# Kernel optimization log

Measured on AMD Instinct MI355X. Metric: run time of the kernel, lower is better.

## Reference

```python
import jax, jax.numpy as jnp
import numpy as np

C_IN = 64
C_QK = C_IN // 8  # 8


def setup_inputs() -> dict:
    key = jax.random.key(0)
    ks = jax.random.split(key, 8)
    B, C, D, H, W = 2, C_IN, 8, 32, 32
    x = jax.random.normal(ks[0], (B, C, D, H, W), dtype=jnp.float32)
    s = 1.0 / np.sqrt(C)
    Wq = jax.random.normal(ks[1], (C_QK, C), dtype=jnp.float32) * s
    bq = jax.random.normal(ks[2], (C_QK,), dtype=jnp.float32) * 0.01
    Wk = jax.random.normal(ks[3], (C_QK, C), dtype=jnp.float32) * s
    bk = jax.random.normal(ks[4], (C_QK,), dtype=jnp.float32) * 0.01
    Wv = jax.random.normal(ks[5], (C, C), dtype=jnp.float32) * s
    bv = jax.random.normal(ks[6], (C,), dtype=jnp.float32) * 0.01
    gamma = jax.random.normal(ks[7], (1,), dtype=jnp.float32) * 0.1
    return {"x": x, "Wq": Wq, "bq": bq, "Wk": Wk, "bk": bk,
            "Wv": Wv, "bv": bv, "gamma": gamma}


def reference(x, Wq, bq, Wk, bk, Wv, bv, gamma):
    B, C, D, H, W = x.shape
    N = D * H * W
    xf = x.reshape(B, C, N)  # flatten spatial dims (D,H,W order)
    # 1x1x1 conv3d == per-position channel matmul
    q = jnp.einsum('oc,bcn->bno', Wq, xf) + bq            # [B, N, Cqk]
    k = jnp.einsum('oc,bcn->bon', Wk, xf) + bk[:, None]   # [B, Cqk, N]
    v = jnp.einsum('oc,bcn->bon', Wv, xf) + bv[:, None]   # [B, C, N]
    energy = jnp.einsum('bnc,bcm->bnm', q, k)             # [B, N, N] (unscaled)
    attn = jax.nn.softmax(energy, axis=-1)
    # out[b,c,m] = sum_n v[b,c,n] * attn[b,m,n]  (bmm with attention^T)
    out = jnp.einsum('bcn,bmn->bcm', v, attn)
    out = out.reshape(B, C, D, H, W)
    return gamma[0] * out + x
```

## Files before the change

### kernel.cpp

```cpp
#include <hip/hip_runtime.h>
#include <hip/hip_bf16.h>
#include <math.h>

#define NPOS 8192
#define CIN 64
#define CQK 8
#define NB 2
#define LOG2E 1.4426950408889634f
#define SOFF 16.0f
#define EXP2_SCALE 8388608.0f
#define EXP2_BIAS  1065173216.0f

typedef __attribute__((ext_vector_type(8))) short bf16x8;
typedef __attribute__((ext_vector_type(16))) float f32x16;

__device__ __forceinline__ unsigned short f2bf(float f) {
  union { float f; unsigned int u; } a; a.f = f;
  unsigned int r = a.u + 0x7FFFu + ((a.u >> 16) & 1u);
  return (unsigned short)(r >> 16);
}

__global__ __launch_bounds__(256, 2) void qkv_proj(
    const float* __restrict__ x,
    const float* __restrict__ Wq, const float* __restrict__ bq,
    const float* __restrict__ Wk, const float* __restrict__ bk,
    const float* __restrict__ Wv, const float* __restrict__ bv,
    unsigned short* __restrict__ Qb, unsigned short* __restrict__ Kb,
    unsigned short* __restrict__ VB) {
  __shared__ float sWq[CQK * CIN], sWk[CQK * CIN], sWv[CIN * CIN], sb[2 * CQK + CIN];
  __shared__ unsigned short sV[32][66];
  int t = threadIdx.x;
  for (int i = t; i < CQK * CIN; i += 256) { sWq[i] = Wq[i] * LOG2E; sWk[i] = Wk[i]; }
  for (int i = t; i < CIN * CIN; i += 256) sWv[i] = Wv[i];
  if (t < CQK) sb[t] = bq[t] * LOG2E;
  if (t >= CQK && t < 2 * CQK) sb[t] = bk[t - CQK];
  if (t >= 2 * CQK && t < 2 * CQK + CIN) sb[t] = bv[t - 2 * CQK];
  __syncthreads();

  int p_loc = t & 31, grp = t >> 5;
  int gid = blockIdx.x * 32 + p_loc;
  int b = gid >> 13;
  int n = gid & (NPOS - 1);
  const float* xp = x + (size_t)b * CIN * NPOS + n;
  float xv[CIN];
#pragma unroll
  for (int c = 0; c < CIN; ++c) xv[c] = xp[(size_t)c * NPOS];

  {
    int o = grp;
    float aq = sb[o], ak = sb[CQK + o];
    const float4* wq4 = (const float4*)&sWq[o * CIN];
    const float4* wk4 = (const float4*)&sWk[o * CIN];
#pragma unroll
    for (int c4 = 0; c4 < 16; ++c4) {
      float4 wq = wq4[c4], wk = wk4[c4];
      float x0 = xv[4 * c4], x1 = xv[4 * c4 + 1], x2 = xv[4 * c4 + 2], x3 = xv[4 * c4 + 3];
      aq += wq.x * x0 + wq.y * x1 + wq.z * x2 + wq.w * x3;
      ak += wk.x * x0 + wk.y * x1 + wk.z * x2 + wk.w * x3;
    }
    Qb[(size_t)gid * CQK + o] = f2bf(aq);
    Kb[(size_t)gid * CQK + o] = f2bf(ak);
  }
#pragma unroll
  for (int oo = 0; oo < 8; ++oo) {
    int o = grp * 8 + oo;
    float av = sb[2 * CQK + o];
    const float4* wv4 = (const float4*)&sWv[o * CIN];
#pragma unroll
    for (int c4 = 0; c4 < 16; ++c4) {
      float4 w = wv4[c4];
      av += w.x * xv[4 * c4] + w.y * xv[4 * c4 + 1] + w.z * xv[4 * c4 + 2] + w.w * xv[4 * c4 + 3];
    }
    sV[p_loc][o] = f2bf(av);
  }
  __syncthreads();

  {
    int gid0 = blockIdx.x * 32;
    int bb = gid0 >> 13;
    int jb = (gid0 & (NPOS - 1)) >> 5;
    int f = t >> 6;
    int ln = t & 63;
    int ch = ((f >> 1) << 5) + (ln & 31);
    int w0 = ((f & 1) << 4) + (((ln >> 5) & 1) << 2);
    union { unsigned short s[8]; bf16x8 v; } ou;
#pragma unroll
    for (int i = 0; i < 8; ++i) {
      int p = w0 + (i & 3) + (((i >> 2) & 1) << 3);
      ou.s[i] = sV[p][ch];
    }
    *reinterpret_cast<bf16x8*>(
        VB + (((size_t)bb * 256 + jb) * 2048 + (size_t)f * 512 + ln * 8)) = ou.v;
  }
}

__global__ __launch_bounds__(512, 2) void flash_attn(
    const unsigned short* __restrict__ Qb, const unsigned short* __restrict__ Kb,
    const unsigned short* __restrict__ VB, const float* __restrict__ x,
    const float* __restrict__ gamma, float* __restrict__ out) {
  int tid = threadIdx.x;
  int wave = tid >> 6, lane = tid & 63;
  int qcol = lane & 31, hi = lane >> 5;
  int blk = blockIdx.x;
  int b = blk >> 7, qt = blk & 127;
  int qbase = qt * 64;

  bf16x8 qfrag0, qfrag1;
#pragma unroll
  for (int i = 0; i < 8; ++i) { qfrag0[i] = 0; qfrag1[i] = 0; }
  if (!hi) {
    qfrag0 = *reinterpret_cast<const bf16x8*>(Qb + ((size_t)b * NPOS + qbase + qcol) * CQK);
    qfrag1 = *reinterpret_cast<const bf16x8*>(Qb + ((size_t)b * NPOS + qbase + 32 + qcol) * CQK);
  }

  bf16x8 ones;
#pragma unroll
  for (int i = 0; i < 8; ++i) ones[i] = (short)0x3F80;

  f32x16 z;
#pragma unroll
  for (int i = 0; i < 16; ++i) z[i] = -SOFF;
  f32x16 accA0, accB0, accA1, accB1;
  f32x16 accL0, accL1;
#pragma unroll
  for (int i = 0; i < 16; ++i) {
    accA0[i] = 0.f; accB0[i] = 0.f; accA1[i] = 0.f; accB1[i] = 0.f;
    accL0[i] = 0.f; accL1[i] = 0.f;
  }

  const unsigned short* Kp = Kb + (size_t)b * NPOS * CQK;
  const bf16x8* Vt = reinterpret_cast<const bf16x8*>(VB + (size_t)b * 256 * 2048);

  int jb0 = wave << 5;
  bf16x8 kcur = *reinterpret_cast<const bf16x8*>(Kp + ((size_t)(jb0 << 5) + qcol) * CQK);

  for (int tt = 0; tt < 32; ++tt) {
    const bf16x8* tile = Vt + (size_t)(jb0 + tt) * 256;
    bf16x8 va0 = tile[lane];
    bf16x8 va1 = tile[64 + lane];
    bf16x8 vb0 = tile[128 + lane];
    bf16x8 vb1 = tile[192 + lane];

    f32x16 S0 = __builtin_amdgcn_mfma_f32_32x32x16_bf16(kcur, qfrag0, z, 0, 0, 0);
    f32x16 S1 = __builtin_amdgcn_mfma_f32_32x32x16_bf16(kcur, qfrag1, z, 0, 0, 0);

    int jn = jb0 + ((tt + 1) & 31);
    bf16x8 knx = *reinterpret_cast<const bf16x8*>(Kp + ((size_t)(jn << 5) + qcol) * CQK);

    unsigned int pk0[8], pk1[8];
#pragma unroll
    for (int jj = 0; jj < 8; ++jj) {
      unsigned int ua = (unsigned int)fmaf(S0[2 * jj],     EXP2_SCALE, EXP2_BIAS);
      unsigned int ub = (unsigned int)fmaf(S0[2 * jj + 1], EXP2_SCALE, EXP2_BIAS);
      unsigned int uc = (unsigned int)fmaf(S1[2 * jj],     EXP2_SCALE, EXP2_BIAS);
      unsigned int ud = (unsigned int)fmaf(S1[2 * jj + 1], EXP2_SCALE, EXP2_BIAS);
      pk0[jj] = __builtin_amdgcn_perm(ub, ua, 0x07060302u);
      pk1[jj] = __builtin_amdgcn_perm(ud, uc, 0x07060302u);
    }

    union { unsigned int ui[4]; bf16x8 v; } PA00, PA10, PA01, PA11;
    PA00.ui[0] = pk0[0]; PA00.ui[1] = pk0[1]; PA00.ui[2] = pk0[2]; PA00.ui[3] = pk0[3];
    PA10.ui[0] = pk0[4]; PA10.ui[1] = pk0[5]; PA10.ui[2] = pk0[6]; PA10.ui[3] = pk0[7];
    PA01.ui[0] = pk1[0]; PA01.ui[1] = pk1[1]; PA01.ui[2] = pk1[2]; PA01.ui[3] = pk1[3];
    PA11.ui[0] = pk1[4]; PA11.ui[1] = pk1[5]; PA11.ui[2] = pk1[6]; PA11.ui[3] = pk1[7];

    accA0 = __builtin_amdgcn_mfma_f32_32x32x16_bf16(va0, PA00.v, accA0, 0, 0, 0);
    accA0 = __builtin_amdgcn_mfma_f32_32x32x16_bf16(va1, PA10.v, accA0, 0, 0, 0);
    accB0 = __builtin_amdgcn_mfma_f32_32x32x16_bf16(vb0, PA00.v, accB0, 0, 0, 0);
    accB0 = __builtin_amdgcn_mfma_f32_32x32x16_bf16(vb1, PA10.v, accB0, 0, 0, 0);
    accA1 = __builtin_amdgcn_mfma_f32_32x32x16_bf16(va0, PA01.v, accA1, 0, 0, 0);
    accA1 = __builtin_amdgcn_mfma_f32_32x32x16_bf16(va1, PA11.v, accA1, 0, 0, 0);
    accB1 = __builtin_amdgcn_mfma_f32_32x32x16_bf16(vb0, PA01.v, accB1, 0, 0, 0);
    accB1 = __builtin_amdgcn_mfma_f32_32x32x16_bf16(vb1, PA11.v, accB1, 0, 0, 0);
    accL0 = __builtin_amdgcn_mfma_f32_32x32x16_bf16(ones, PA00.v, accL0, 0, 0, 0);
    accL0 = __builtin_amdgcn_mfma_f32_32x32x16_bf16(ones, PA10.v, accL0, 0, 0, 0);
    accL1 = __builtin_amdgcn_mfma_f32_32x32x16_bf16(ones, PA01.v, accL1, 0, 0, 0);
    accL1 = __builtin_amdgcn_mfma_f32_32x32x16_bf16(ones, PA11.v, accL1, 0, 0, 0);

    kcur = knx;
  }

  __shared__ float sL[8][64];
  __shared__ float sLinv[64];
  __shared__ float sacc[64][68];
  if (!hi) { sL[wave][qcol] = accL0[0]; sL[wave][32 + qcol] = accL1[0]; }
  __syncthreads();
  if (tid < 64) {
    float L = 0.f;
#pragma unroll
    for (int w2 = 0; w2 < 8; ++w2) L += sL[w2][tid];
    sLinv[tid] = 1.0f / L;
  }

  for (int w2 = 0; w2 < 8; ++w2) {
    __syncthreads();
    if (wave == w2) {
#pragma unroll
      for (int k = 0; k < 4; ++k) {
        int c0 = (k << 3) + (hi << 2);
        float4 cA0 = make_float4(accA0[4 * k], accA0[4 * k + 1], accA0[4 * k + 2], accA0[4 * k + 3]);
        float4 cB0 = make_float4(accB0[4 * k], accB0[4 * k + 1], accB0[4 * k + 2], accB0[4 * k + 3]);
        float4 cA1 = make_float4(accA1[4 * k], accA1[4 * k + 1], accA1[4 * k + 2], accA1[4 * k + 3]);
        float4 cB1 = make_float4(accB1[4 * k], accB1[4 * k + 1], accB1[4 * k + 2], accB1[4 * k + 3]);
        float4* pA0 = (float4*)&sacc[qcol][c0];
        float4* pB0 = (float4*)&sacc[qcol][c0 + 32];
        float4* pA1 = (float4*)&sacc[32 + qcol][c0];
        float4* pB1 = (float4*)&sacc[32 + qcol][c0 + 32];
        if (w2 == 0) { *pA0 = cA0; *pB0 = cB0; *pA1 = cA1; *pB1 = cB1; }
        else {
          float4 a = *pA0, bb = *pB0, c = *pA1, d = *pB1;
          a.x += cA0.x; a.y += cA0.y; a.z += cA0.z; a.w += cA0.w;
          bb.x += cB0.x; bb.y += cB0.y; bb.z += cB0.z; bb.w += cB0.w;
          c.x += cA1.x; c.y += cA1.y; c.z += cA1.z; c.w += cA1.w;
          d.x += cB1.x; d.y += cB1.y; d.z += cB1.z; d.w += cB1.w;
          *pA0 = a; *pB0 = bb; *pA1 = c; *pB1 = d;
        }
      }
    }
  }
  __syncthreads();

  float g = gamma[0];
  for (int i = tid; i < CIN * 64; i += 512) {
    int c = i >> 6, q = i & 63;
    size_t idx = ((size_t)b * CIN + c) * NPOS + qbase + q;
    out[idx] = g * sacc[q][c] * sLinv[q] + x[idx];
  }
}

extern "C" void kernel_launch(void* const* d_in, const int* in_sizes, int n_in,
                              void* d_out, int out_size, void* d_ws, size_t ws_size,
                              hipStream_t stream) {
  const float* x     = (const float*)d_in[0];
  const float* Wq    = (const float*)d_in[1];
  const float* bq    = (const float*)d_in[2];
  const float* Wk    = (const float*)d_in[3];
  const float* bk    = (const float*)d_in[4];
  const float* Wv    = (const float*)d_in[5];
  const float* bv    = (const float*)d_in[6];
  const float* gamma = (const float*)d_in[7];
  float* out = (float*)d_out;

  unsigned short* Qb = (unsigned short*)d_ws;
  unsigned short* Kb = Qb + (size_t)NB * NPOS * CQK;
  unsigned short* VB = Kb + (size_t)NB * NPOS * CQK;

  qkv_proj<<<dim3(NB * NPOS / 32), dim3(256), 0, stream>>>(
      x, Wq, bq, Wk, bk, Wv, bv, Qb, Kb, VB);
  flash_attn<<<dim3(NB * NPOS / 64), dim3(512), 0, stream>>>(
      Qb, Kb, VB, x, gamma, out);
}
```

Baseline: 46.21 us.

## Double-buffer V tile loads two iterations ahead and use hardware exp2

Prefetches V tiles two iterations ahead into a rotating register pipeline so global load latency overlaps with the MFMA work, and unrolls the loop by two. It also replaces the bit-trick exp2 approximation (fma into the float exponent field) with the hardware exp2 instruction. The row-sum MFMAs are moved ahead of the PV MFMAs. The cost is higher register pressure from the extra V buffers, which could hurt occupancy under launch_bounds(256,2), plus more transcendental-unit instructions per tile.

```diff
diff --git a/kernel.cpp b/kernel.cpp
--- a/kernel.cpp
+++ b/kernel.cpp
@@ -8,8 +8,6 @@
 #define NB 2
 #define LOG2E 1.4426950408889634f
 #define SOFF 16.0f
-#define EXP2_SCALE 8388608.0f
-#define EXP2_BIAS  1065173216.0f
 
 typedef __attribute__((ext_vector_type(8))) short bf16x8;
 typedef __attribute__((ext_vector_type(16))) float f32x16;
@@ -134,28 +132,33 @@
   int jb0 = wave << 5;
   bf16x8 kcur = *reinterpret_cast<const bf16x8*>(Kp + ((size_t)(jb0 << 5) + qcol) * CQK);
 
+  const bf16x8* tp0 = Vt + (size_t)jb0 * 256;
+  const bf16x8* tp1 = Vt + (size_t)(jb0 + 1) * 256;
+  bf16x8 vc0 = tp0[lane],       vc1 = tp0[64 + lane];
+  bf16x8 vc2 = tp0[128 + lane], vc3 = tp0[192 + lane];
+  bf16x8 vn0 = tp1[lane],       vn1 = tp1[64 + lane];
+  bf16x8 vn2 = tp1[128 + lane], vn3 = tp1[192 + lane];
+
+#pragma unroll 2
   for (int tt = 0; tt < 32; ++tt) {
-    const bf16x8* tile = Vt + (size_t)(jb0 + tt) * 256;
-    bf16x8 va0 = tile[lane];
-    bf16x8 va1 = tile[64 + lane];
-    bf16x8 vb0 = tile[128 + lane];
-    bf16x8 vb1 = tile[192 + lane];
-
     f32x16 S0 = __builtin_amdgcn_mfma_f32_32x32x16_bf16(kcur, qfrag0, z, 0, 0, 0);
     f32x16 S1 = __builtin_amdgcn_mfma_f32_32x32x16_bf16(kcur, qfrag1, z, 0, 0, 0);
 
-    int jn = jb0 + ((tt + 1) & 31);
-    bf16x8 knx = *reinterpret_cast<const bf16x8*>(Kp + ((size_t)(jn << 5) + qcol) * CQK);
+    const bf16x8* tile2 = Vt + (size_t)(jb0 + ((tt + 2) & 31)) * 256;
+    bf16x8 w0 = tile2[lane],       w1 = tile2[64 + lane];
+    bf16x8 w2 = tile2[128 + lane], w3 = tile2[192 + lane];
+    bf16x8 knx = *reinterpret_cast<const bf16x8*>(
+        Kp + ((size_t)((jb0 + ((tt + 1) & 31)) << 5) + qcol) * CQK);
 
     unsigned int pk0[8], pk1[8];
 #pragma unroll
     for (int jj = 0; jj < 8; ++jj) {
-      unsigned int ua = (unsigned int)fmaf(S0[2 * jj],     EXP2_SCALE, EXP2_BIAS);
-      unsigned int ub = (unsigned int)fmaf(S0[2 * jj + 1], EXP2_SCALE, EXP2_BIAS);
-      unsigned int uc = (unsigned int)fmaf(S1[2 * jj],     EXP2_SCALE, EXP2_BIAS);
-      unsigned int ud = (unsigned int)fmaf(S1[2 * jj + 1], EXP2_SCALE, EXP2_BIAS);
-      pk0[jj] = __builtin_amdgcn_perm(ub, ua, 0x07060302u);
-      pk1[jj] = __builtin_amdgcn_perm(ud, uc, 0x07060302u);
+      float pa = __builtin_amdgcn_exp2f(S0[2 * jj]);
+      float pb = __builtin_amdgcn_exp2f(S0[2 * jj + 1]);
+      float pc = __builtin_amdgcn_exp2f(S1[2 * jj]);
+      float pd = __builtin_amdgcn_exp2f(S1[2 * jj + 1]);
+      pk0[jj] = __builtin_amdgcn_perm(__float_as_uint(pb), __float_as_uint(pa), 0x07060302u);
+      pk1[jj] = __builtin_amdgcn_perm(__float_as_uint(pd), __float_as_uint(pc), 0x07060302u);
     }
 
     union { unsigned int ui[4]; bf16x8 v; } PA00, PA10, PA01, PA11;
@@ -164,19 +167,22 @@
     PA01.ui[0] = pk1[0]; PA01.ui[1] = pk1[1]; PA01.ui[2] = pk1[2]; PA01.ui[3] = pk1[3];
     PA11.ui[0] = pk1[4]; PA11.ui[1] = pk1[5]; PA11.ui[2] = pk1[6]; PA11.ui[3] = pk1[7];
 
-    accA0 = __builtin_amdgcn_mfma_f32_32x32x16_bf16(va0, PA00.v, accA0, 0, 0, 0);
-    accA0 = __builtin_amdgcn_mfma_f32_32x32x16_bf16(va1, PA10.v, accA0, 0, 0, 0);
-    accB0 = __builtin_amdgcn_mfma_f32_32x32x16_bf16(vb0, PA00.v, accB0, 0, 0, 0);
-    accB0 = __builtin_amdgcn_mfma_f32_32x32x16_bf16(vb1, PA10.v, accB0, 0, 0, 0);
-    accA1 = __builtin_amdgcn_mfma_f32_32x32x16_bf16(va0, PA01.v, accA1, 0, 0, 0);
-    accA1 = __builtin_amdgcn_mfma_f32_32x32x16_bf16(va1, PA11.v, accA1, 0, 0, 0);
-    accB1 = __builtin_amdgcn_mfma_f32_32x32x16_bf16(vb0, PA01.v, accB1, 0, 0, 0);
-    accB1 = __builtin_amdgcn_mfma_f32_32x32x16_bf16(vb1, PA11.v, accB1, 0, 0, 0);
     accL0 = __builtin_amdgcn_mfma_f32_32x32x16_bf16(ones, PA00.v, accL0, 0, 0, 0);
     accL0 = __builtin_amdgcn_mfma_f32_32x32x16_bf16(ones, PA10.v, accL0, 0, 0, 0);
     accL1 = __builtin_amdgcn_mfma_f32_32x32x16_bf16(ones, PA01.v, accL1, 0, 0, 0);
     accL1 = __builtin_amdgcn_mfma_f32_32x32x16_bf16(ones, PA11.v, accL1, 0, 0, 0);
 
+    accA0 = __builtin_amdgcn_mfma_f32_32x32x16_bf16(vc0, PA00.v, accA0, 0, 0, 0);
+    accA0 = __builtin_amdgcn_mfma_f32_32x32x16_bf16(vc1, PA10.v, accA0, 0, 0, 0);
+    accB0 = __builtin_amdgcn_mfma_f32_32x32x16_bf16(vc2, PA00.v, accB0, 0, 0, 0);
+    accB0 = __builtin_amdgcn_mfma_f32_32x32x16_bf16(vc3, PA10.v, accB0, 0, 0, 0);
+    accA1 = __builtin_amdgcn_mfma_f32_32x32x16_bf16(vc0, PA01.v, accA1, 0, 0, 0);
+    accA1 = __builtin_amdgcn_mfma_f32_32x32x16_bf16(vc1, PA11.v, accA1, 0, 0, 0);
+    accB1 = __builtin_amdgcn_mfma_f32_32x32x16_bf16(vc2, PA01.v, accB1, 0, 0, 0);
+    accB1 = __builtin_amdgcn_mfma_f32_32x32x16_bf16(vc3, PA11.v, accB1, 0, 0, 0);
+
+    vc0 = vn0; vc1 = vn1; vc2 = vn2; vc3 = vn3;
+    vn0 = w0;  vn1 = w1;  vn2 = w2;  vn3 = w3;
     kcur = knx;
   }
 
```

Result: no change. 45.72 us (-1.1%).
